# Optimization experiments

Measured on AMD Instinct MI355X. Metric: run time of the kernel, lower is better.

## Reference

```python
import jax, jax.numpy as jnp
import numpy as np

TOP_K = 2
NEG_INF = -1.0e9
EPS = 1e-12

def setup_inputs() -> dict:
    key = jax.random.key(0)
    k1, k2, k3 = jax.random.split(key, 3)
    N, D, EMB, E = 65536, 2048, 256, 64
    x = jax.random.normal(k1, (N, D), dtype=jnp.float32)
    W_proj = jax.random.normal(k2, (D, EMB), dtype=jnp.float32) * (1.0 / np.sqrt(D))
    expert_emb = jax.random.normal(k3, (EMB, E), dtype=jnp.float32) * (1.0 / np.sqrt(EMB))
    temperature = jnp.ones((1,), dtype=jnp.float32)
    return {"x": x, "W_proj": W_proj, "expert_emb": expert_emb, "temperature": temperature}

def _l2norm(v, axis):
    return v / jnp.sqrt(jnp.sum(v * v, axis=axis, keepdims=True) + EPS)

def reference(x, W_proj, expert_emb, temperature):
    # [N, EMB] projection, then dual L2-normalize -> cosine similarities [N, E]
    proj = x @ W_proj
    proj_n = _l2norm(proj, axis=-1)
    emb_n = _l2norm(expert_emb, axis=0)
    cos = proj_n @ emb_n                      # [N, E]
    logits = cos * temperature[0]
    # top-k selection -> one-hot mask -> masked softmax
    top_v, top_i = jax.lax.top_k(logits, TOP_K)   # [N, k]
    N = logits.shape[0]
    rows = jnp.arange(N)[:, None]
    mask = jnp.zeros_like(logits).at[rows, top_i].set(1.0)
    masked_logits = jnp.where(mask > 0, logits, NEG_INF)
    expert_weights = jax.nn.softmax(masked_logits, axis=-1)  # [N, E]
    raw_gate_probs = jax.nn.softmax(logits, axis=-1)
    # auxiliary_info: (gate_logits, cosine_similarities, raw_gate_probs)
    return expert_weights, top_i.astype(jnp.int32), logits, cos, raw_gate_probs
```

## Files before the change

kernel.cpp:

```cpp
#include <hip/hip_runtime.h>

#define N_ROWS 65536
#define DIM    2048
#define EMBD   256
#define NEXP   64
#define BMAIN  64
#define EPSN   1e-12f
#define TAU    5e-4f
#define CAP    8192
#define RPB    4

#define WS_EINV   65536
#define WS_WPACK  131072
#define WS_EPACK  (131072 + 2097152)

typedef short short8 __attribute__((ext_vector_type(8)));
typedef float f32x4 __attribute__((ext_vector_type(4)));
typedef unsigned short ushort_t;

__device__ __forceinline__ ushort_t f2bf(float v) {
  unsigned u = __float_as_uint(v);
  u += 0x7fffu + ((u >> 16) & 1u);
  return (ushort_t)(u >> 16);
}
__device__ __forceinline__ float bf2f(ushort_t h) {
  return __uint_as_float((unsigned)h << 16);
}

__device__ __forceinline__ void top3_insert(float w, int j,
                                            float& v1, int& i1,
                                            float& v2, int& i2,
                                            float& v3, int& i3) {
  bool b1 = (w > v1) || (w == v1 && j < i1);
  bool b2 = (w > v2) || (w == v2 && j < i2);
  bool b3 = (w > v3) || (w == v3 && j < i3);
  if (b1)      { v3 = v2; i3 = i2; v2 = v1; i2 = i1; v1 = w; i1 = j; }
  else if (b2) { v3 = v2; i3 = i2; v2 = w;  i2 = j; }
  else if (b3) { v3 = w;  i3 = j; }
}

__device__ __forceinline__ void top2_insert_d(double w, int j,
                                              double& v1, int& i1,
                                              double& v2, int& i2) {
  bool b1 = (w > v1) || (w == v1 && j < i1);
  bool b2 = (w > v2) || (w == v2 && j < i2);
  if (b1) { v2 = v1; i2 = i1; v1 = w; i1 = j; }
  else if (b2) { v2 = w; i2 = j; }
}

__global__ __launch_bounds__(256)
void prep_norms(const float* __restrict__ emb, char* __restrict__ ws) {
  __shared__ float part[4][64];
  const int tid = threadIdx.x;
  const int e = tid & 63, p = tid >> 6;
  float s = 0.f;
  for (int m = p * 64; m < p * 64 + 64; ++m) {
    float v = emb[m * NEXP + e];
    s += v * v;
  }
  part[p][e] = s;
  __syncthreads();
  if (tid < 64) {
    float* einv = (float*)(ws + WS_EINV);
    einv[tid] = 1.0f / sqrtf(part[0][tid] + part[1][tid] + part[2][tid] +
                             part[3][tid] + EPSN);
  }
}

__global__ __launch_bounds__(256)
void prep_pack(const float* __restrict__ Wp, const float* __restrict__ emb,
               char* __restrict__ ws) {
  const int gid = blockIdx.x * 256 + threadIdx.x;
  if (blockIdx.x < 256) {
    short8* wH = (short8*)(ws + WS_WPACK);
    short8* wL = wH + 65536;
    const int l = gid & 63, s = (gid >> 6) & 63, t = gid >> 12;
    short8 hv, lv;
    #pragma unroll
    for (int j = 0; j < 8; ++j) {
      float v = Wp[(size_t)(32 * s + ((l >> 4) << 3) + j) * EMBD + 16 * t + (l & 15)];
      ushort_t h = f2bf(v);
      hv[j] = (short)h;
      lv[j] = (short)f2bf(v - bf2f(h));
    }
    wH[(t * 64 + s) * 64 + l] = hv;
    wL[(t * 64 + s) * 64 + l] = lv;
  } else {
    const int g2 = gid - 65536;
    const int l = g2 & 63, s2 = (g2 >> 6) & 7, nt = g2 >> 9;
    const float* einv = (const float*)(ws + WS_EINV);
    short8* eH = (short8*)(ws + WS_EPACK);
    short8* eL = eH + 2048;
    short8 hv, lv;
    #pragma unroll
    for (int j = 0; j < 8; ++j) {
      int k = 32 * s2 + ((l >> 4) << 3) + j;
      int n = 16 * nt + (l & 15);
      float v = emb[k * NEXP + n] * einv[n];
      ushort_t h = f2bf(v);
      hv[j] = (short)h;
      lv[j] = (short)f2bf(v - bf2f(h));
    }
    eH[(nt * 8 + s2) * 64 + l] = hv;
    eL[(nt * 8 + s2) * 64 + l] = lv;
  }
}

__global__ __launch_bounds__(256, 3)
void gate_main(const float* __restrict__ x, const float* __restrict__ temp,
               float* __restrict__ out, char* __restrict__ ws) {
  __shared__ union {
    struct { ushort_t AH[4][64][8]; ushort_t AL[4][64][8]; } a;
    float cb[32][68];
  } u;
  __shared__ ushort_t PH[2][8][64][8];
  __shared__ ushort_t PL[2][8][64][8];
  __shared__ float sPart[4][64];
  __shared__ float sInv[64];

  const int tid  = threadIdx.x;
  const int lane = tid & 63;
  const int w    = tid >> 6;
  const int lm   = lane & 15;
  const int lq   = lane >> 4;
  const int n0   = blockIdx.x * BMAIN;

  const short8* wH = (const short8*)(ws + WS_WPACK);
  const short8* wL = wH + 65536;
  const short8* eH = (const short8*)(ws + WS_EPACK);
  const short8* eL = eH + 2048;
  int* flag = (int*)ws;

  f32x4 acc[4][4];
  #pragma unroll
  for (int i = 0; i < 4; ++i)
    #pragma unroll
    for (int j = 0; j < 4; ++j) acc[i][j] = (f32x4){0.f, 0.f, 0.f, 0.f};

  const int arow = tid >> 2;
  const int achk = tid & 3;
  const float4* xld = (const float4*)(x + (size_t)(n0 + arow) * DIM + achk * 8);
  ushort_t* ah = &u.a.AH[arow >> 4][(arow & 15) + 16 * achk][0];
  ushort_t* al = &u.a.AL[arow >> 4][(arow & 15) + 16 * achk][0];

  for (int s = 0; s < 64; ++s) {
    float4 xa = xld[8 * s];
    float4 xb = xld[8 * s + 1];
    __syncthreads();
    {
      float v[8] = {xa.x, xa.y, xa.z, xa.w, xb.x, xb.y, xb.z, xb.w};
      short8 hv, lv;
      #pragma unroll
      for (int j = 0; j < 8; ++j) {
        ushort_t h = f2bf(v[j]);
        hv[j] = (short)h;
        lv[j] = (short)f2bf(v[j] - bf2f(h));
      }
      *(short8*)ah = hv;
      *(short8*)al = lv;
    }
    __syncthreads();
    short8 Bh[4], Bl[4];
    #pragma unroll
    for (int nt = 0; nt < 4; ++nt) {
      const int t = 4 * w + nt;
      Bh[nt] = wH[(t * 64 + s) * 64 + lane];
      Bl[nt] = wL[(t * 64 + s) * 64 + lane];
    }
    short8 Af[4];
    #pragma unroll
    for (int mt = 0; mt < 4; ++mt) Af[mt] = *(const short8*)&u.a.AH[mt][lane][0];
    #pragma unroll
    for (int mt = 0; mt < 4; ++mt)
      #pragma unroll
      for (int nt = 0; nt < 4; ++nt) {
        acc[mt][nt] = __builtin_amdgcn_mfma_f32_16x16x32_bf16(Af[mt], Bh[nt], acc[mt][nt], 0, 0, 0);
        acc[mt][nt] = __builtin_amdgcn_mfma_f32_16x16x32_bf16(Af[mt], Bl[nt], acc[mt][nt], 0, 0, 0);
      }
    #pragma unroll
    for (int mt = 0; mt < 4; ++mt) Af[mt] = *(const short8*)&u.a.AL[mt][lane][0];
    #pragma unroll
    for (int mt = 0; mt < 4; ++mt)
      #pragma unroll
      for (int nt = 0; nt < 4; ++nt)
        acc[mt][nt] = __builtin_amdgcn_mfma_f32_16x16x32_bf16(Af[mt], Bh[nt], acc[mt][nt], 0, 0, 0);
  }

  #pragma unroll
  for (int mt = 0; mt < 4; ++mt) {
    #pragma unroll
    for (int reg = 0; reg < 4; ++reg) {
      float ssum = 0.f;
      #pragma unroll
      for (int nt = 0; nt < 4; ++nt) {
        float v = acc[mt][nt][reg];
        ssum += v * v;
      }
      #pragma unroll
      for (int off = 1; off < 16; off <<= 1) ssum += __shfl_xor(ssum, off, 16);
      if (lm == 0) sPart[w][mt * 16 + lq * 4 + reg] = ssum;
    }
  }
  __syncthreads();
  if (tid < 64)
    sInv[tid] = 1.0f / sqrtf(sPart[0][tid] + sPart[1][tid] + sPart[2][tid] +
                             sPart[3][tid] + EPSN);
  __syncthreads();

  const float T = temp[0];
  float* o_w   = out;
  float* o_idx = out + (size_t)N_ROWS * 64;
  float* o_lg  = o_idx + (size_t)N_ROWS * 2;
  float* o_cos = o_lg + (size_t)N_ROWS * 64;
  float* o_rp  = o_cos + (size_t)N_ROWS * 64;

  for (int h = 0; h < 2; ++h) {
    #pragma unroll
    for (int mt = 2 * h; mt < 2 * h + 2; ++mt) {
      #pragma unroll
      for (int nt = 0; nt < 4; ++nt) {
        #pragma unroll
        for (int reg = 0; reg < 4; ++reg) {
          const int row = mt * 16 + lq * 4 + reg;
          const int col = w * 64 + nt * 16 + lm;
          float p = acc[mt][nt][reg] * sInv[row];
          ushort_t hi = f2bf(p);
          ushort_t lo = f2bf(p - bf2f(hi));
          const int rr = row - 32 * h;
          const int li = (rr & 15) + 16 * ((col >> 3) & 3);
          PH[rr >> 4][col >> 5][li][col & 7] = hi;
          PL[rr >> 4][col >> 5][li][col & 7] = lo;
        }
      }
    }
    __syncthreads();
    f32x4 a2[2];
    a2[0] = (f32x4){0.f, 0.f, 0.f, 0.f};
    a2[1] = (f32x4){0.f, 0.f, 0.f, 0.f};
    for (int s2 = 0; s2 < 8; ++s2) {
      short8 bh = eH[(w * 8 + s2) * 64 + lane];
      short8 bl = eL[(w * 8 + s2) * 64 + lane];
      #pragma unroll
      for (int m2 = 0; m2 < 2; ++m2) {
        short8 ph = *(const short8*)&PH[m2][s2][lane][0];
        short8 pl = *(const short8*)&PL[m2][s2][lane][0];
        a2[m2] = __builtin_amdgcn_mfma_f32_16x16x32_bf16(ph, bh, a2[m2], 0, 0, 0);
        a2[m2] = __builtin_amdgcn_mfma_f32_16x16x32_bf16(ph, bl, a2[m2], 0, 0, 0);
        a2[m2] = __builtin_amdgcn_mfma_f32_16x16x32_bf16(pl, bh, a2[m2], 0, 0, 0);
      }
    }
    #pragma unroll
    for (int m2 = 0; m2 < 2; ++m2)
      #pragma unroll
      for (int reg = 0; reg < 4; ++reg)
        u.cb[m2 * 16 + lq * 4 + reg][w * 16 + lm] = a2[m2][reg];
    __syncthreads();

    if (tid < 128) {
      const int r  = tid >> 2;
      const int qq = tid & 3;
      float cs[16], lg[16];
      #pragma unroll
      for (int i = 0; i < 4; ++i) {
        float4 cv = *(const float4*)&u.cb[r][16 * qq + 4 * i];
        cs[4*i+0] = cv.x; cs[4*i+1] = cv.y; cs[4*i+2] = cv.z; cs[4*i+3] = cv.w;
      }
      #pragma unroll
      for (int j = 0; j < 16; ++j) lg[j] = cs[j] * T;
      float v1 = -3e38f, v2 = -3e38f, v3 = -3e38f;
      int   i1 = 1 << 30, i2 = 1 << 30, i3 = 1 << 30;
      #pragma unroll
      for (int j = 0; j < 16; ++j)
        top3_insert(lg[j], 16 * qq + j, v1, i1, v2, i2, v3, i3);
      #pragma unroll
      for (int off = 1; off < 4; off <<= 1) {
        float w1 = __shfl_xor(v1, off, 4); int j1 = __shfl_xor(i1, off, 4);
        float w2 = __shfl_xor(v2, off, 4); int j2 = __shfl_xor(i2, off, 4);
        float w3 = __shfl_xor(v3, off, 4); int j3 = __shfl_xor(i3, off, 4);
        top3_insert(w1, j1, v1, i1, v2, i2, v3, i3);
        top3_insert(w2, j2, v1, i1, v2, i2, v3, i3);
        top3_insert(w3, j3, v1, i1, v2, i2, v3, i3);
      }
      float ex[16], ssum = 0.f;
      #pragma unroll
      for (int j = 0; j < 16; ++j) { ex[j] = expf(lg[j] - v1); ssum += ex[j]; }
      #pragma unroll
      for (int off = 1; off < 4; off <<= 1) ssum += __shfl_xor(ssum, off, 4);

      const int n = n0 + 32 * h + r;
      const float e21 = expf(v2 - v1);
      const float dm  = 1.0f / (1.0f + e21);
      const size_t ob = (size_t)n * 64 + 16 * qq;
      #pragma unroll
      for (int i = 0; i < 4; ++i) {
        float t4[4], r4[4];
        #pragma unroll
        for (int jj = 0; jj < 4; ++jj) {
          int e = 16 * qq + 4 * i + jj;
          t4[jj] = (e == i1) ? dm : ((e == i2) ? e21 * dm : 0.f);
          r4[jj] = ex[4 * i + jj] / ssum;
        }
        *(float4*)&o_w[ob + 4 * i]   = make_float4(t4[0], t4[1], t4[2], t4[3]);
        *(float4*)&o_rp[ob + 4 * i]  = make_float4(r4[0], r4[1], r4[2], r4[3]);
        *(float4*)&o_lg[ob + 4 * i]  = make_float4(lg[4*i], lg[4*i+1], lg[4*i+2], lg[4*i+3]);
        *(float4*)&o_cos[ob + 4 * i] = make_float4(cs[4*i], cs[4*i+1], cs[4*i+2], cs[4*i+3]);
      }
      if (qq == 0) {
        o_idx[(size_t)n * 2]     = (float)i1;
        o_idx[(size_t)n * 2 + 1] = (float)i2;
        if ((v1 - v2 < TAU) || (v2 - v3 < TAU)) {
          int slot = atomicAdd(&flag[0], 1);
          if (slot < CAP) flag[4 + slot] = n;
        }
      }
    }
    __syncthreads();
  }
}

__global__ __launch_bounds__(256)
void refine_kernel(const float* __restrict__ x,
                   const float* __restrict__ Wp,
                   const float* __restrict__ emb,
                   const float* __restrict__ temp,
                   float* __restrict__ out,
                   const int* __restrict__ ws) {
  __shared__ float  xs[RPB][DIM];
  __shared__ double projd[RPB][EMBD];
  __shared__ double embinv[NEXP];
  __shared__ double red[256];

  const int tid = threadIdx.x;
  int cnt = ws[0];
  if (cnt > CAP) cnt = CAP;
  const int base = blockIdx.x * RPB;
  if (base >= cnt) return;
  const int nr = min(RPB, cnt - base);
  int rows[RPB];
  #pragma unroll
  for (int j = 0; j < RPB; ++j) rows[j] = ws[4 + base + (j < nr ? j : 0)];

  {
    const int e = tid & 63, part = tid >> 6;
    double s = 0.0;
    for (int m = part * 64; m < part * 64 + 64; ++m) {
      double v = (double)emb[m * NEXP + e];
      s += v * v;
    }
    red[tid] = s;
  }
  __syncthreads();
  if (tid < 64)
    embinv[tid] = 1.0 / sqrt(red[tid] + red[tid + 64] + red[tid + 128] +
                             red[tid + 192] + 1e-12);

  for (int j = 0; j < nr; ++j)
    for (int k = tid; k < DIM; k += 256)
      xs[j][k] = x[(size_t)rows[j] * DIM + k];
  __syncthreads();

  {
    double s[RPB];
    #pragma unroll
    for (int j = 0; j < RPB; ++j) s[j] = 0.0;
    for (int k = 0; k < DIM; ++k) {
      double wv = (double)Wp[(size_t)k * EMBD + tid];
      #pragma unroll
      for (int j = 0; j < RPB; ++j) s[j] += (double)xs[j][k] * wv;
    }
    #pragma unroll
    for (int j = 0; j < RPB; ++j) projd[j][tid] = s[j];
  }
  __syncthreads();

  if (tid < 64) {
    float* o_w   = out;
    float* o_idx = out + (size_t)N_ROWS * 64;
    float* o_lg  = o_idx + (size_t)N_ROWS * 2;
    float* o_cos = o_lg + (size_t)N_ROWS * 64;
    float* o_rp  = o_cos + (size_t)N_ROWS * 64;
    const double T = (double)temp[0];
    const int e = tid;
    for (int j = 0; j < nr; ++j) {
      const int row = rows[j];
      double q = 0.0;
      #pragma unroll
      for (int p = 0; p < 4; ++p) {
        double v = projd[j][e + 64 * p];
        q += v * v;
      }
      #pragma unroll
      for (int off = 1; off < 64; off <<= 1) q += __shfl_xor(q, off, 64);
      const double invn = 1.0 / sqrt(q + 1e-12);
      double c = 0.0;
      for (int m = 0; m < EMBD; ++m)
        c += projd[j][m] * (double)emb[m * NEXP + e];
      c *= invn * embinv[e];
      const double lg = c * T;

      double v1 = lg, v2 = -1.0e300;
      int   i1 = e,  i2 = 1 << 30;
      #pragma unroll
      for (int off = 1; off < 64; off <<= 1) {
        double w1 = __shfl_xor(v1, off, 64); int j1 = __shfl_xor(i1, off, 64);
        double w2 = __shfl_xor(v2, off, 64); int j2 = __shfl_xor(i2, off, 64);
        top2_insert_d(w1, j1, v1, i1, v2, i2);
        top2_insert_d(w2, j2, v1, i1, v2, i2);
      }
      const double ex = exp(lg - v1);
      double ssum = ex;
      #pragma unroll
      for (int off = 1; off < 64; off <<= 1) ssum += __shfl_xor(ssum, off, 64);
      const double e21 = exp(v2 - v1);
      const double dm  = 1.0 / (1.0 + e21);

      const size_t ob = (size_t)row * 64 + e;
      o_w[ob]   = (e == i1) ? (float)dm : ((e == i2) ? (float)(e21 * dm) : 0.0f);
      o_lg[ob]  = (float)lg;
      o_cos[ob] = (float)c;
      o_rp[ob]  = (float)(ex / ssum);
      if (e == 0) {
        o_idx[(size_t)row * 2]     = (float)i1;
        o_idx[(size_t)row * 2 + 1] = (float)i2;
      }
    }
  }
}

extern "C" void kernel_launch(void* const* d_in, const int* in_sizes, int n_in,
                              void* d_out, int out_size, void* d_ws, size_t ws_size,
                              hipStream_t stream) {
  const float* x    = (const float*)d_in[0];
  const float* Wp   = (const float*)d_in[1];
  const float* emb  = (const float*)d_in[2];
  const float* temp = (const float*)d_in[3];
  float* out = (float*)d_out;
  char* ws = (char*)d_ws;
  (void)in_sizes; (void)n_in; (void)out_size; (void)ws_size;

  hipMemsetAsync(d_ws, 0, 64, stream);
  prep_norms<<<dim3(1), dim3(256), 0, stream>>>(emb, ws);
  prep_pack<<<dim3(264), dim3(256), 0, stream>>>(Wp, emb, ws);
  gate_main<<<dim3(N_ROWS / BMAIN), dim3(256), 0, stream>>>(x, temp, out, ws);
  refine_kernel<<<dim3(CAP / RPB), dim3(256), 0, stream>>>(
      x, Wp, emb, temp, out, (const int*)ws);
}
```

Before: 2.175 ms.

## Double-buffer A tiles, swizzle LDS, stream B fragments, parallelize fixup kernel

The main GEMM loop now double-buffers the bf16 hi/lo A tiles in shared memory. The next x chunk is loaded and converted while MFMAs run on the current buffer, which removes one barrier per iteration. LDS slots are XOR-swizzled to reduce bank conflicts, and B fragments are loaded one nt ahead instead of all four at once to reduce register pressure; MFMA sections also get raised wave priority. The fp64 fixup kernel gains vectorized x loads, an unrolled projection loop, and a cosine dot product split across all 256 threads with a shared-memory reduction, at the cost of extra barriers.

After: 2.053 ms. 1.06x faster.

```diff
diff --git a/kernel.cpp b/kernel.cpp
--- a/kernel.cpp
+++ b/kernel.cpp
@@ -25,6 +25,17 @@
 }
 __device__ __forceinline__ float bf2f(ushort_t h) {
   return __uint_as_float((unsigned)h << 16);
+}
+
+__device__ __forceinline__ void cvt8(const float4 a, const float4 b,
+                                     short8& hv, short8& lv) {
+  float v[8] = {a.x, a.y, a.z, a.w, b.x, b.y, b.z, b.w};
+  #pragma unroll
+  for (int j = 0; j < 8; ++j) {
+    ushort_t h = f2bf(v[j]);
+    hv[j] = (short)h;
+    lv[j] = (short)f2bf(v[j] - bf2f(h));
+  }
 }
 
 __device__ __forceinline__ void top3_insert(float w, int j,
@@ -106,11 +117,15 @@
   }
 }
 
+__device__ __forceinline__ int aswz(int idx) {
+  return idx ^ (((idx >> 4) & 3) << 1);
+}
+
 __global__ __launch_bounds__(256, 3)
 void gate_main(const float* __restrict__ x, const float* __restrict__ temp,
                float* __restrict__ out, char* __restrict__ ws) {
-  __shared__ union {
-    struct { ushort_t AH[4][64][8]; ushort_t AL[4][64][8]; } a;
+  __shared__ alignas(16) union {
+    struct { ushort_t AH[2][4][64][8]; ushort_t AL[2][4][64][8]; } a;
     float cb[32][68];
   } u;
   __shared__ ushort_t PH[2][8][64][8];
@@ -140,50 +155,60 @@
   const int arow = tid >> 2;
   const int achk = tid & 3;
   const float4* xld = (const float4*)(x + (size_t)(n0 + arow) * DIM + achk * 8);
-  ushort_t* ah = &u.a.AH[arow >> 4][(arow & 15) + 16 * achk][0];
-  ushort_t* al = &u.a.AL[arow >> 4][(arow & 15) + 16 * achk][0];
+  const int mtW   = arow >> 4;
+  const int slotW = aswz((arow & 15) + 16 * achk);
+  const int slotR = aswz(lane);
+
+  {
+    float4 xa = xld[0];
+    float4 xb = xld[1];
+    short8 hv, lv;
+    cvt8(xa, xb, hv, lv);
+    *(short8*)&u.a.AH[0][mtW][slotW][0] = hv;
+    *(short8*)&u.a.AL[0][mtW][slotW][0] = lv;
+  }
+  __syncthreads();
 
   for (int s = 0; s < 64; ++s) {
-    float4 xa = xld[8 * s];
-    float4 xb = xld[8 * s + 1];
-    __syncthreads();
-    {
-      float v[8] = {xa.x, xa.y, xa.z, xa.w, xb.x, xb.y, xb.z, xb.w};
+    const int cur = s & 1;
+    const int sn = (s < 63) ? s + 1 : 63;
+    float4 nxa = xld[8 * sn];
+    float4 nxb = xld[8 * sn + 1];
+
+    short8 AfH[4], AfL[4];
+    #pragma unroll
+    for (int mt = 0; mt < 4; ++mt) {
+      AfH[mt] = *(const short8*)&u.a.AH[cur][mt][slotR][0];
+      AfL[mt] = *(const short8*)&u.a.AL[cur][mt][slotR][0];
+    }
+
+    short8 Bh = wH[((4 * w) * 64 + s) * 64 + lane];
+    short8 Bl = wL[((4 * w) * 64 + s) * 64 + lane];
+    __builtin_amdgcn_s_setprio(1);
+    #pragma unroll
+    for (int nt = 0; nt < 4; ++nt) {
+      short8 Bh2, Bl2;
+      if (nt < 3) {
+        Bh2 = wH[((4 * w + nt + 1) * 64 + s) * 64 + lane];
+        Bl2 = wL[((4 * w + nt + 1) * 64 + s) * 64 + lane];
+      }
+      #pragma unroll
+      for (int mt = 0; mt < 4; ++mt) {
+        acc[mt][nt] = __builtin_amdgcn_mfma_f32_16x16x32_bf16(AfH[mt], Bh, acc[mt][nt], 0, 0, 0);
+        acc[mt][nt] = __builtin_amdgcn_mfma_f32_16x16x32_bf16(AfH[mt], Bl, acc[mt][nt], 0, 0, 0);
+        acc[mt][nt] = __builtin_amdgcn_mfma_f32_16x16x32_bf16(AfL[mt], Bh, acc[mt][nt], 0, 0, 0);
+      }
+      Bh = Bh2; Bl = Bl2;
+    }
+    __builtin_amdgcn_s_setprio(0);
+
+    if (s < 63) {
       short8 hv, lv;
-      #pragma unroll
-      for (int j = 0; j < 8; ++j) {
-        ushort_t h = f2bf(v[j]);
-        hv[j] = (short)h;
-        lv[j] = (short)f2bf(v[j] - bf2f(h));
-      }
-      *(short8*)ah = hv;
-      *(short8*)al = lv;
-    }
-    __syncthreads();
-    short8 Bh[4], Bl[4];
-    #pragma unroll
-    for (int nt = 0; nt < 4; ++nt) {
-      const int t = 4 * w + nt;
-      Bh[nt] = wH[(t * 64 + s) * 64 + lane];
-      Bl[nt] = wL[(t * 64 + s) * 64 + lane];
-    }
-    short8 Af[4];
-    #pragma unroll
-    for (int mt = 0; mt < 4; ++mt) Af[mt] = *(const short8*)&u.a.AH[mt][lane][0];
-    #pragma unroll
-    for (int mt = 0; mt < 4; ++mt)
-      #pragma unroll
-      for (int nt = 0; nt < 4; ++nt) {
-        acc[mt][nt] = __builtin_amdgcn_mfma_f32_16x16x32_bf16(Af[mt], Bh[nt], acc[mt][nt], 0, 0, 0);
-        acc[mt][nt] = __builtin_amdgcn_mfma_f32_16x16x32_bf16(Af[mt], Bl[nt], acc[mt][nt], 0, 0, 0);
-      }
-    #pragma unroll
-    for (int mt = 0; mt < 4; ++mt) Af[mt] = *(const short8*)&u.a.AL[mt][lane][0];
-    #pragma unroll
-    for (int mt = 0; mt < 4; ++mt)
-      #pragma unroll
-      for (int nt = 0; nt < 4; ++nt)
-        acc[mt][nt] = __builtin_amdgcn_mfma_f32_16x16x32_bf16(Af[mt], Bh[nt], acc[mt][nt], 0, 0, 0);
+      cvt8(nxa, nxb, hv, lv);
+      *(short8*)&u.a.AH[cur ^ 1][mtW][slotW][0] = hv;
+      *(short8*)&u.a.AL[cur ^ 1][mtW][slotW][0] = lv;
+    }
+    __syncthreads();
   }
 
   #pragma unroll
@@ -355,34 +380,55 @@
                              red[tid + 192] + 1e-12);
 
   for (int j = 0; j < nr; ++j)
-    for (int k = tid; k < DIM; k += 256)
-      xs[j][k] = x[(size_t)rows[j] * DIM + k];
+    for (int k = tid * 4; k < DIM; k += 1024)
+      *(float4*)&xs[j][k] = *(const float4*)&x[(size_t)rows[j] * DIM + k];
   __syncthreads();
 
   {
     double s[RPB];
     #pragma unroll
     for (int j = 0; j < RPB; ++j) s[j] = 0.0;
-    for (int k = 0; k < DIM; ++k) {
-      double wv = (double)Wp[(size_t)k * EMBD + tid];
-      #pragma unroll
-      for (int j = 0; j < RPB; ++j) s[j] += (double)xs[j][k] * wv;
+    #pragma unroll 2
+    for (int k = 0; k < DIM; k += 4) {
+      double w0 = (double)Wp[(size_t)(k + 0) * EMBD + tid];
+      double w1 = (double)Wp[(size_t)(k + 1) * EMBD + tid];
+      double w2 = (double)Wp[(size_t)(k + 2) * EMBD + tid];
+      double w3 = (double)Wp[(size_t)(k + 3) * EMBD + tid];
+      #pragma unroll
+      for (int j = 0; j < RPB; ++j) {
+        float4 xv = *(const float4*)&xs[j][k];
+        s[j] += (double)xv.x * w0;
+        s[j] += (double)xv.y * w1;
+        s[j] += (double)xv.z * w2;
+        s[j] += (double)xv.w * w3;
+      }
     }
     #pragma unroll
     for (int j = 0; j < RPB; ++j) projd[j][tid] = s[j];
   }
   __syncthreads();
 
-  if (tid < 64) {
-    float* o_w   = out;
-    float* o_idx = out + (size_t)N_ROWS * 64;
-    float* o_lg  = o_idx + (size_t)N_ROWS * 2;
-    float* o_cos = o_lg + (size_t)N_ROWS * 64;
-    float* o_rp  = o_cos + (size_t)N_ROWS * 64;
-    const double T = (double)temp[0];
-    const int e = tid;
-    for (int j = 0; j < nr; ++j) {
+  float* o_w   = out;
+  float* o_idx = out + (size_t)N_ROWS * 64;
+  float* o_lg  = o_idx + (size_t)N_ROWS * 2;
+  float* o_cos = o_lg + (size_t)N_ROWS * 64;
+  float* o_rp  = o_cos + (size_t)N_ROWS * 64;
+  const double T = (double)temp[0];
+  const int e  = tid & 63;
+  const int pp = tid >> 6;
+
+  for (int j = 0; j < nr; ++j) {
+    double c0 = 0.0, c1 = 0.0;
+    for (int m = 64 * pp; m < 64 * pp + 64; m += 2) {
+      c0 += projd[j][m]     * (double)emb[m * NEXP + e];
+      c1 += projd[j][m + 1] * (double)emb[(m + 1) * NEXP + e];
+    }
+    red[tid] = c0 + c1;
+    __syncthreads();
+
+    if (tid < 64) {
       const int row = rows[j];
+      double c = red[e] + red[e + 64] + red[e + 128] + red[e + 192];
       double q = 0.0;
       #pragma unroll
       for (int p = 0; p < 4; ++p) {
@@ -392,9 +438,6 @@
       #pragma unroll
       for (int off = 1; off < 64; off <<= 1) q += __shfl_xor(q, off, 64);
       const double invn = 1.0 / sqrt(q + 1e-12);
-      double c = 0.0;
-      for (int m = 0; m < EMBD; ++m)
-        c += projd[j][m] * (double)emb[m * NEXP + e];
       c *= invn * embinv[e];
       const double lg = c * T;
 
@@ -424,6 +467,7 @@
         o_idx[(size_t)row * 2 + 1] = (float)i2;
       }
     }
+    __syncthreads();
   }
 }
 
```
